# Optimization experiments

Hardware: AMD Instinct MI355X
Metric: run time of the kernel (lower is better)

## Reference

```python
import jax, jax.numpy as jnp
import numpy as np

N_NODES = 50000
N_EDGES = 1600000
F_IN = 32
F_OUT = 32


def setup_inputs() -> dict:
    key = jax.random.key(0)
    k1, k2, k3, k4, k5 = jax.random.split(key, 5)
    inputs = jax.random.normal(k1, (N_EDGES, F_IN), dtype=jnp.float32)
    src = jax.random.randint(k2, (N_EDGES,), 0, N_NODES, dtype=jnp.int32)
    dst = jax.random.randint(k3, (N_EDGES,), 0, N_NODES, dtype=jnp.int32)
    W = jax.random.normal(k4, (F_OUT, F_IN), dtype=jnp.float32) * (1.0 / np.sqrt(F_IN))
    b = jax.random.normal(k5, (F_OUT,), dtype=jnp.float32) * 0.01
    return {"inputs": inputs, "src": src, "dst": dst, "W": W, "b": b}


def reference(inputs, src, dst, W, b):
    # Step 1: node h = mean of incoming edge features (mean over in-edges).
    ones = jnp.ones((inputs.shape[0],), dtype=inputs.dtype)
    in_deg = jax.ops.segment_sum(ones, dst, num_segments=N_NODES)  # [N]
    node_sum = jax.ops.segment_sum(inputs, dst, num_segments=N_NODES)  # [N, F]
    node_mean = node_sum / jnp.maximum(in_deg, 1.0)[:, None]
    # Step 2: send_and_recv: msg = src node h; reduce = sum at dst node.
    node_h = jax.ops.segment_sum(node_mean[src], dst, num_segments=N_NODES)  # [N, F]
    # Step 3: edge h = mean of its two endpoint node features.
    edge_h = 0.5 * (node_h[src] + node_h[dst])  # [E, F]
    # Step 4: final linear projection on edge features.
    return edge_h @ W.T + b
```

## Files before the change

kernel.cpp:

```cpp
#include <hip/hip_runtime.h>

#define N_NODES 50000
#define N_EDGES 1600000
#define F 32
#define BSH 7
#define BSIZE (1 << BSH)
#define NB ((N_NODES + BSIZE - 1) >> BSH)
#define FILL_CHUNK 4096
#define EMASK 0x1FFFFF

typedef float f4 __attribute__((ext_vector_type(4)));
typedef _Float16 h4 __attribute__((ext_vector_type(4)));

__device__ __forceinline__ f4 nt_load4(const float* p) {
    return __builtin_nontemporal_load((const f4*)p);
}
__device__ __forceinline__ int nt_loadi(const int* p) {
    return __builtin_nontemporal_load(p);
}

__global__ __launch_bounds__(256)
void k_bhist(const int* __restrict__ dst, int* __restrict__ bhist) {
    __shared__ int lh[NB];
    for (int i = threadIdx.x; i < NB; i += 256) lh[i] = 0;
    __syncthreads();
    for (int e = blockIdx.x * blockDim.x + threadIdx.x; e < N_EDGES;
         e += gridDim.x * blockDim.x)
        atomicAdd(&lh[dst[e] >> BSH], 1);
    __syncthreads();
    for (int i = threadIdx.x; i < NB; i += 256)
        if (lh[i]) atomicAdd(&bhist[i], lh[i]);
}

__global__ __launch_bounds__(512)
void k_bscan(const int* __restrict__ bhist,
             int* __restrict__ bucket_off,
             int* __restrict__ cursor) {
    __shared__ int s[512];
    int t = threadIdx.x;
    int v = (t < NB) ? bhist[t] : 0;
    s[t] = v;
    __syncthreads();
    for (int off = 1; off < 512; off <<= 1) {
        int u = (t >= off) ? s[t - off] : 0;
        __syncthreads();
        s[t] += u;
        __syncthreads();
    }
    if (t < NB) {
        int ex = s[t] - v;
        bucket_off[t] = ex;
        cursor[t] = ex;
    }
    if (t == NB - 1) bucket_off[NB] = s[t];
}

__global__ __launch_bounds__(256)
void k_coarse_fill(const int* __restrict__ dst,
                   const int* __restrict__ src,
                   int* __restrict__ cursor,
                   int* __restrict__ coarseE,
                   unsigned short* __restrict__ coarseS) {
    __shared__ int lh[NB];
    __shared__ int gb[NB];
    int lo = blockIdx.x * FILL_CHUNK;
    int hi = min(lo + FILL_CHUNK, N_EDGES);

    for (int i = threadIdx.x; i < NB; i += 256) lh[i] = 0;
    __syncthreads();
    for (int e = lo + threadIdx.x; e < hi; e += 256)
        atomicAdd(&lh[dst[e] >> BSH], 1);
    __syncthreads();
    for (int i = threadIdx.x; i < NB; i += 256) {
        gb[i] = atomicAdd(&cursor[i], lh[i]);
        lh[i] = 0;
    }
    __syncthreads();
    for (int e = lo + threadIdx.x; e < hi; e += 256) {
        int d = dst[e];
        int bk = d >> BSH;
        int r = atomicAdd(&lh[bk], 1);
        int p = gb[bk] + r;
        coarseE[p] = e | ((d & (BSIZE - 1)) << 21);
        coarseS[p] = (unsigned short)src[e];
    }
}

__global__ __launch_bounds__(256)
void k_exact_fill(const int* __restrict__ coarseE,
                  const unsigned short* __restrict__ coarseS,
                  const int* __restrict__ bucket_off,
                  int* __restrict__ row_off,
                  int* __restrict__ eid_sorted,
                  unsigned short* __restrict__ src_sorted) {
    __shared__ int cnt[BSIZE];
    __shared__ int s[BSIZE];
    __shared__ int cur[BSIZE];
    int tid = threadIdx.x;
    int b = blockIdx.x;
    int lo = bucket_off[b], hi = bucket_off[b + 1];

    if (tid < BSIZE) cnt[tid] = 0;
    __syncthreads();
    for (int i = lo + tid; i < hi; i += 256)
        atomicAdd(&cnt[(coarseE[i] >> 21) & (BSIZE - 1)], 1);
    __syncthreads();
    if (tid < BSIZE) s[tid] = cnt[tid];
    __syncthreads();
    for (int off = 1; off < BSIZE; off <<= 1) {
        int v = 0;
        if (tid < BSIZE && tid >= off) v = s[tid - off];
        __syncthreads();
        if (tid < BSIZE) s[tid] += v;
        __syncthreads();
    }
    int nbase = b << BSH;
    if (tid < BSIZE) {
        int base = lo + s[tid] - cnt[tid];
        cur[tid] = base;
        if (nbase + tid < N_NODES) row_off[nbase + tid] = base;
    }
    if (b == NB - 1 && tid == 0) row_off[N_NODES] = N_EDGES;
    __syncthreads();
    for (int i = lo + tid; i < hi; i += 256) {
        int ev = coarseE[i];
        int l = (ev >> 21) & (BSIZE - 1);
        int p = atomicAdd(&cur[l], 1);
        eid_sorted[p] = ev & EMASK;
        src_sorted[p] = coarseS[i];
    }
}

__global__ __launch_bounds__(256)
void k_node_mean(const float* __restrict__ inputs,
                 const int* __restrict__ eid_sorted,
                 const int* __restrict__ row_off,
                 _Float16* __restrict__ node_mean) {
    int wave = (blockIdx.x * blockDim.x + threadIdx.x) >> 6;
    if (wave >= N_NODES) return;
    int lane  = threadIdx.x & 63;
    int eslot = lane >> 3;
    int q     = lane & 7;

    int s0 = row_off[wave];
    int s1 = row_off[wave + 1];

    f4 acc = {0.f, 0.f, 0.f, 0.f};
    int i = s0 + eslot;
    int e = (i < s1) ? eid_sorted[i] : 0;
    while (i < s1) {
        int inext = i + 8;
        int enext = (inext < s1) ? eid_sorted[inext] : 0;
        f4 v = nt_load4(&inputs[(size_t)e * F + q * 4]);
        acc += v;
        i = inext; e = enext;
    }
    #pragma unroll
    for (int m = 8; m <= 32; m <<= 1) {
        acc.x += __shfl_xor(acc.x, m);
        acc.y += __shfl_xor(acc.y, m);
        acc.z += __shfl_xor(acc.z, m);
        acc.w += __shfl_xor(acc.w, m);
    }
    if (eslot == 0) {
        float r = 1.0f / fmaxf((float)(s1 - s0), 1.0f);
        f4 o = acc * r;
        *reinterpret_cast<h4*>(&node_mean[(size_t)wave * F + q * 4]) =
            __builtin_convertvector(o, h4);
    }
}

__global__ __launch_bounds__(256)
void k_node_h_project(const unsigned short* __restrict__ src_sorted,
                      const int* __restrict__ row_off,
                      const _Float16* __restrict__ node_mean,
                      const float* __restrict__ W,
                      _Float16* __restrict__ node_p) {
    __shared__ float Wl[32][33];
    __shared__ float hr[4][36];

    int tid = threadIdx.x;
    #pragma unroll
    for (int i = tid; i < 1024; i += 256) Wl[i >> 5][i & 31] = W[i];

    int wv    = tid >> 6;
    int lane  = tid & 63;
    int eslot = lane >> 3;
    int q     = lane & 7;
    int n     = blockIdx.x * 4 + wv;

    int s0 = row_off[n];
    int s1 = row_off[n + 1];

    f4 acc = {0.f, 0.f, 0.f, 0.f};
    int i = s0 + eslot;
    int s = (i < s1) ? (int)src_sorted[i] : 0;
    while (i < s1) {
        int inext = i + 8;
        int snext = (inext < s1) ? (int)src_sorted[inext] : 0;
        h4 v = *reinterpret_cast<const h4*>(&node_mean[(size_t)s * F + q * 4]);
        acc += __builtin_convertvector(v, f4);
        i = inext; s = snext;
    }
    #pragma unroll
    for (int m = 8; m <= 32; m <<= 1) {
        acc.x += __shfl_xor(acc.x, m);
        acc.y += __shfl_xor(acc.y, m);
        acc.z += __shfl_xor(acc.z, m);
        acc.w += __shfl_xor(acc.w, m);
    }
    if (eslot == 0) {
        *reinterpret_cast<f4*>(&hr[wv][q * 4]) = acc;
    }
    __syncthreads();

    if (tid < 128) {
        int ln = tid >> 5;
        int o  = tid & 31;
        float sacc = 0.f;
        #pragma unroll
        for (int i2 = 0; i2 < 32; ++i2) sacc += hr[ln][i2] * Wl[o][i2];
        node_p[(size_t)(blockIdx.x * 4 + ln) * F + o] = (_Float16)sacc;
    }
}

__global__ __launch_bounds__(256)
void k_edge_out(const int* __restrict__ src,
                const int* __restrict__ dst,
                const _Float16* __restrict__ node_p,
                const float* __restrict__ b,
                float* __restrict__ out) {
    int tid = blockIdx.x * blockDim.x + threadIdx.x;
    if (tid >= N_EDGES * 8) return;
    int e = tid >> 3;
    int q = tid & 7;
    int s = nt_loadi(&src[e]);
    int d = nt_loadi(&dst[e]);

    h4 ah = *reinterpret_cast<const h4*>(&node_p[(size_t)s * F + q * 4]);
    h4 ch = *reinterpret_cast<const h4*>(&node_p[(size_t)d * F + q * 4]);
    const f4 a  = __builtin_convertvector(ah, f4);
    const f4 c  = __builtin_convertvector(ch, f4);
    const f4 bb = *reinterpret_cast<const f4*>(&b[q * 4]);

    f4 r = 0.5f * (a + c) + bb;
    __builtin_nontemporal_store(r, (f4*)&out[(size_t)e * F + q * 4]);
}

extern "C" void kernel_launch(void* const* d_in, const int* in_sizes, int n_in,
                              void* d_out, int out_size, void* d_ws, size_t ws_size,
                              hipStream_t stream) {
    const float* inputs = (const float*)d_in[0];
    const int*   src    = (const int*)d_in[1];
    const int*   dst    = (const int*)d_in[2];
    const float* W      = (const float*)d_in[3];
    const float* b      = (const float*)d_in[4];
    float* out = (float*)d_out;

    int*  coarseE    = (int*)d_ws;
    int*  eid_sorted = coarseE + N_EDGES;
    int*  bhist      = eid_sorted + N_EDGES;
    int*  bucket_off = bhist + NB;
    int*  cursor     = bucket_off + NB + 1;
    int*  row_off    = cursor + NB;
    _Float16* node_mean = (_Float16*)(row_off + N_NODES + 1);
    _Float16* node_p    = node_mean + (size_t)N_NODES * F;
    unsigned short* coarseS    = (unsigned short*)(node_p + (size_t)N_NODES * F);
    unsigned short* src_sorted = coarseS + N_EDGES;

    hipMemsetAsync(bhist, 0, NB * sizeof(int), stream);

    k_bhist<<<512, 256, 0, stream>>>(dst, bhist);
    k_bscan<<<1, 512, 0, stream>>>(bhist, bucket_off, cursor);
    k_coarse_fill<<<(N_EDGES + FILL_CHUNK - 1) / FILL_CHUNK, 256, 0, stream>>>(
        dst, src, cursor, coarseE, coarseS);
    k_exact_fill<<<NB, 256, 0, stream>>>(
        coarseE, coarseS, bucket_off, row_off, eid_sorted, src_sorted);

    int node_blocks = (N_NODES + 3) / 4;
    k_node_mean<<<node_blocks, 256, 0, stream>>>(inputs, eid_sorted, row_off, node_mean);
    k_node_h_project<<<N_NODES / 4, 256, 0, stream>>>(
        src_sorted, row_off, node_mean, W, node_p);
    k_edge_out<<<(N_EDGES * 8 + 255) / 256, 256, 0, stream>>>(src, dst, node_p, b, out);
}
```

Baseline: 237.7 us.

## Scatter fp16 edge rows during coarse bucketing and fuse exact sort with node mean

The coarse fill pass now also streams each edge's input row, converts it to fp16 and scatters it into a bucket-ordered buffer. A fused bucket kernel then does the fine sort, writes row offsets and src_sorted, and computes node means from the bucket-local rows through a shared-memory permutation. The random per-edge gathers of fp32 input rows and the eid_sorted array go away, and the bucket size is halved to 64 nodes. In exchange, scattered fp16 row writes and an extra 100MB buffer round trip are added. Buckets with more than WCAP edges would overflow the shared permutation and produce wrong means.

```diff
diff --git a/kernel.cpp b/kernel.cpp
--- a/kernel.cpp
+++ b/kernel.cpp
@@ -3,11 +3,12 @@
 #define N_NODES 50000
 #define N_EDGES 1600000
 #define F 32
-#define BSH 7
+#define BSH 6
 #define BSIZE (1 << BSH)
 #define NB ((N_NODES + BSIZE - 1) >> BSH)
-#define FILL_CHUNK 4096
-#define EMASK 0x1FFFFF
+#define CHUNK 2048
+#define NCHUNK ((N_EDGES + CHUNK - 1) / CHUNK)
+#define WCAP 2560
 
 typedef float f4 __attribute__((ext_vector_type(4)));
 typedef _Float16 h4 __attribute__((ext_vector_type(4)));
@@ -32,16 +33,16 @@
         if (lh[i]) atomicAdd(&bhist[i], lh[i]);
 }
 
-__global__ __launch_bounds__(512)
+__global__ __launch_bounds__(1024)
 void k_bscan(const int* __restrict__ bhist,
              int* __restrict__ bucket_off,
              int* __restrict__ cursor) {
-    __shared__ int s[512];
+    __shared__ int s[1024];
     int t = threadIdx.x;
     int v = (t < NB) ? bhist[t] : 0;
     s[t] = v;
     __syncthreads();
-    for (int off = 1; off < 512; off <<= 1) {
+    for (int off = 1; off < 1024; off <<= 1) {
         int u = (t >= off) ? s[t - off] : 0;
         __syncthreads();
         s[t] += u;
@@ -56,117 +57,127 @@
 }
 
 __global__ __launch_bounds__(256)
-void k_coarse_fill(const int* __restrict__ dst,
+void k_coarse_rows(const int* __restrict__ dst,
                    const int* __restrict__ src,
+                   const float* __restrict__ inputs,
                    int* __restrict__ cursor,
                    int* __restrict__ coarseE,
-                   unsigned short* __restrict__ coarseS) {
+                   _Float16* __restrict__ coarseR) {
     __shared__ int lh[NB];
     __shared__ int gb[NB];
-    int lo = blockIdx.x * FILL_CHUNK;
-    int hi = min(lo + FILL_CHUNK, N_EDGES);
+    __shared__ unsigned int ds[CHUNK];
+    int lo = blockIdx.x * CHUNK;
+    int hi = min(lo + CHUNK, N_EDGES);
 
     for (int i = threadIdx.x; i < NB; i += 256) lh[i] = 0;
     __syncthreads();
-    for (int e = lo + threadIdx.x; e < hi; e += 256)
-        atomicAdd(&lh[dst[e] >> BSH], 1);
+    for (int e = lo + threadIdx.x; e < hi; e += 256) {
+        int d = dst[e];
+        ds[e - lo] = ((unsigned)d << 16) | (unsigned)src[e];
+        atomicAdd(&lh[d >> BSH], 1);
+    }
     __syncthreads();
     for (int i = threadIdx.x; i < NB; i += 256) {
         gb[i] = atomicAdd(&cursor[i], lh[i]);
         lh[i] = 0;
     }
     __syncthreads();
-    for (int e = lo + threadIdx.x; e < hi; e += 256) {
-        int d = dst[e];
-        int bk = d >> BSH;
-        int r = atomicAdd(&lh[bk], 1);
-        int p = gb[bk] + r;
-        coarseE[p] = e | ((d & (BSIZE - 1)) << 21);
-        coarseS[p] = (unsigned short)src[e];
-    }
-}
-
-__global__ __launch_bounds__(256)
-void k_exact_fill(const int* __restrict__ coarseE,
-                  const unsigned short* __restrict__ coarseS,
-                  const int* __restrict__ bucket_off,
-                  int* __restrict__ row_off,
-                  int* __restrict__ eid_sorted,
-                  unsigned short* __restrict__ src_sorted) {
+
+    int lane  = threadIdx.x & 63;
+    int wv    = threadIdx.x >> 6;
+    int eslot = lane >> 3;
+    int q     = lane & 7;
+    for (int base = lo + wv * 8; base < hi; base += 32) {
+        int e = base + eslot;
+        bool valid = e < hi;
+        int p = 0;
+        if (valid && q == 0) {
+            unsigned v = ds[e - lo];
+            int d = (int)(v >> 16);
+            int bk = d >> BSH;
+            int r = atomicAdd(&lh[bk], 1);
+            p = gb[bk] + r;
+            coarseE[p] = ((d & (BSIZE - 1)) << 16) | (int)(v & 0xFFFFu);
+        }
+        p = __shfl(p, eslot * 8);
+        if (valid) {
+            f4 x = nt_load4(&inputs[(size_t)e * F + q * 4]);
+            *reinterpret_cast<h4*>(&coarseR[((size_t)p << 5) + q * 4]) =
+                __builtin_convertvector(x, h4);
+        }
+    }
+}
+
+__global__ __launch_bounds__(512)
+void k_bucket_mean(const int* __restrict__ coarseE,
+                   const int* __restrict__ bucket_off,
+                   const _Float16* __restrict__ coarseR,
+                   int* __restrict__ row_off,
+                   unsigned short* __restrict__ src_sorted,
+                   _Float16* __restrict__ node_mean) {
     __shared__ int cnt[BSIZE];
-    __shared__ int s[BSIZE];
+    __shared__ int sloc[BSIZE + 1];
     __shared__ int cur[BSIZE];
+    __shared__ unsigned short perm[WCAP];
+
     int tid = threadIdx.x;
     int b = blockIdx.x;
-    int lo = bucket_off[b], hi = bucket_off[b + 1];
+    int wlo = bucket_off[b], whi = bucket_off[b + 1];
+    int n_e = whi - wlo;
 
     if (tid < BSIZE) cnt[tid] = 0;
     __syncthreads();
-    for (int i = lo + tid; i < hi; i += 256)
-        atomicAdd(&cnt[(coarseE[i] >> 21) & (BSIZE - 1)], 1);
-    __syncthreads();
-    if (tid < BSIZE) s[tid] = cnt[tid];
-    __syncthreads();
-    for (int off = 1; off < BSIZE; off <<= 1) {
-        int v = 0;
-        if (tid < BSIZE && tid >= off) v = s[tid - off];
-        __syncthreads();
-        if (tid < BSIZE) s[tid] += v;
-        __syncthreads();
-    }
+    for (int i = tid; i < n_e; i += 512)
+        atomicAdd(&cnt[coarseE[wlo + i] >> 16], 1);
+    __syncthreads();
+    if (tid == 0) {
+        int run = 0;
+        #pragma unroll
+        for (int k = 0; k < BSIZE; ++k) { sloc[k] = run; run += cnt[k]; }
+        sloc[BSIZE] = run;
+    }
+    __syncthreads();
     int nbase = b << BSH;
     if (tid < BSIZE) {
-        int base = lo + s[tid] - cnt[tid];
-        cur[tid] = base;
-        if (nbase + tid < N_NODES) row_off[nbase + tid] = base;
+        cur[tid] = sloc[tid];
+        if (nbase + tid < N_NODES) row_off[nbase + tid] = wlo + sloc[tid];
     }
     if (b == NB - 1 && tid == 0) row_off[N_NODES] = N_EDGES;
     __syncthreads();
-    for (int i = lo + tid; i < hi; i += 256) {
-        int ev = coarseE[i];
-        int l = (ev >> 21) & (BSIZE - 1);
+    for (int i = tid; i < n_e; i += 512) {
+        int id = coarseE[wlo + i];
+        int l = id >> 16;
         int p = atomicAdd(&cur[l], 1);
-        eid_sorted[p] = ev & EMASK;
-        src_sorted[p] = coarseS[i];
-    }
-}
-
-__global__ __launch_bounds__(256)
-void k_node_mean(const float* __restrict__ inputs,
-                 const int* __restrict__ eid_sorted,
-                 const int* __restrict__ row_off,
-                 _Float16* __restrict__ node_mean) {
-    int wave = (blockIdx.x * blockDim.x + threadIdx.x) >> 6;
-    if (wave >= N_NODES) return;
-    int lane  = threadIdx.x & 63;
-    int eslot = lane >> 3;
-    int q     = lane & 7;
-
-    int s0 = row_off[wave];
-    int s1 = row_off[wave + 1];
-
-    f4 acc = {0.f, 0.f, 0.f, 0.f};
-    int i = s0 + eslot;
-    int e = (i < s1) ? eid_sorted[i] : 0;
-    while (i < s1) {
-        int inext = i + 8;
-        int enext = (inext < s1) ? eid_sorted[inext] : 0;
-        f4 v = nt_load4(&inputs[(size_t)e * F + q * 4]);
-        acc += v;
-        i = inext; e = enext;
-    }
-    #pragma unroll
-    for (int m = 8; m <= 32; m <<= 1) {
-        acc.x += __shfl_xor(acc.x, m);
-        acc.y += __shfl_xor(acc.y, m);
-        acc.z += __shfl_xor(acc.z, m);
-        acc.w += __shfl_xor(acc.w, m);
-    }
-    if (eslot == 0) {
-        float r = 1.0f / fmaxf((float)(s1 - s0), 1.0f);
-        f4 o = acc * r;
-        *reinterpret_cast<h4*>(&node_mean[(size_t)wave * F + q * 4]) =
-            __builtin_convertvector(o, h4);
+        if (p < WCAP) perm[p] = (unsigned short)i;
+        src_sorted[wlo + p] = (unsigned short)(id & 0xFFFF);
+    }
+    __syncthreads();
+
+    int wv = tid >> 6, lane = tid & 63, eslot = lane >> 3, q = lane & 7;
+    for (int k = 0; k < 8; ++k) {
+        int n = wv * 8 + k;
+        if (nbase + n >= N_NODES) break;
+        int a0 = sloc[n], a1 = sloc[n + 1];
+        f4 acc = {0.f, 0.f, 0.f, 0.f};
+        for (int i = a0 + eslot; i < a1; i += 8) {
+            int widx = perm[i];
+            h4 v = *reinterpret_cast<const h4*>(
+                &coarseR[((size_t)(wlo + widx) << 5) + q * 4]);
+            acc += __builtin_convertvector(v, f4);
+        }
+        #pragma unroll
+        for (int m = 8; m <= 32; m <<= 1) {
+            acc.x += __shfl_xor(acc.x, m);
+            acc.y += __shfl_xor(acc.y, m);
+            acc.z += __shfl_xor(acc.z, m);
+            acc.w += __shfl_xor(acc.w, m);
+        }
+        if (eslot == 0) {
+            float r = 1.0f / fmaxf((float)(a1 - a0), 1.0f);
+            f4 o = acc * r;
+            *reinterpret_cast<h4*>(&node_mean[(size_t)(nbase + n) * F + q * 4]) =
+                __builtin_convertvector(o, h4);
+        }
     }
 }
 
@@ -258,27 +269,26 @@
     float* out = (float*)d_out;
 
     int*  coarseE    = (int*)d_ws;
-    int*  eid_sorted = coarseE + N_EDGES;
-    int*  bhist      = eid_sorted + N_EDGES;
+    int*  bhist      = coarseE + N_EDGES;
     int*  bucket_off = bhist + NB;
     int*  cursor     = bucket_off + NB + 1;
     int*  row_off    = cursor + NB;
-    _Float16* node_mean = (_Float16*)(row_off + N_NODES + 1);
+    size_t ihead = (size_t)N_EDGES + 3 * NB + 1 + N_NODES + 1;
+    ihead = (ihead + 3) & ~(size_t)3;
+    _Float16* coarseR   = (_Float16*)((int*)d_ws + ihead);
+    _Float16* node_mean = coarseR + (size_t)N_EDGES * F;
     _Float16* node_p    = node_mean + (size_t)N_NODES * F;
-    unsigned short* coarseS    = (unsigned short*)(node_p + (size_t)N_NODES * F);
-    unsigned short* src_sorted = coarseS + N_EDGES;
+    unsigned short* src_sorted =
+        (unsigned short*)(node_p + (size_t)N_NODES * F);
 
     hipMemsetAsync(bhist, 0, NB * sizeof(int), stream);
 
     k_bhist<<<512, 256, 0, stream>>>(dst, bhist);
-    k_bscan<<<1, 512, 0, stream>>>(bhist, bucket_off, cursor);
-    k_coarse_fill<<<(N_EDGES + FILL_CHUNK - 1) / FILL_CHUNK, 256, 0, stream>>>(
-        dst, src, cursor, coarseE, coarseS);
-    k_exact_fill<<<NB, 256, 0, stream>>>(
-        coarseE, coarseS, bucket_off, row_off, eid_sorted, src_sorted);
-
-    int node_blocks = (N_NODES + 3) / 4;
-    k_node_mean<<<node_blocks, 256, 0, stream>>>(inputs, eid_sorted, row_off, node_mean);
+    k_bscan<<<1, 1024, 0, stream>>>(bhist, bucket_off, cursor);
+    k_coarse_rows<<<NCHUNK, 256, 0, stream>>>(
+        dst, src, inputs, cursor, coarseE, coarseR);
+    k_bucket_mean<<<NB, 512, 0, stream>>>(
+        coarseE, bucket_off, coarseR, row_off, src_sorted, node_mean);
     k_node_h_project<<<N_NODES / 4, 256, 0, stream>>>(
         src_sorted, row_off, node_mean, W, node_p);
     k_edge_out<<<(N_EDGES * 8 + 255) / 256, 256, 0, stream>>>(src, dst, node_p, b, out);
```

Result: slower. 288.9 us (+21.5%).
